# Performance work log

Hardware: AMD Instinct MI355X
Metric: run time of the kernel (lower is better)

Reference implementation:

```python
import jax, jax.numpy as jnp
import numpy as np

TEMPERATURE = 0.07
EPS = 1e-12  # matches torch F.normalize default eps


def setup_inputs() -> dict:
    key = jax.random.key(0)
    k1, k2 = jax.random.split(key)
    N, D = 4096, 768
    z1 = jax.random.normal(k1, (N, D), dtype=jnp.float32)
    z2 = jax.random.normal(k2, (N, D), dtype=jnp.float32)
    return {"z1": z1, "z2": z2}


def reference(z1, z2):
    # L2-normalize each row (torch.F.normalize with eps clamp)
    def l2norm(x):
        n = jnp.linalg.norm(x, axis=1, keepdims=True)
        return x / jnp.maximum(n, EPS)

    z1 = l2norm(z1)
    z2 = l2norm(z2)
    z = jnp.concatenate([z1, z2], axis=0)          # [2N, D]
    N2 = z.shape[0]
    N = N2 // 2

    sim = jnp.matmul(z, z.T) / TEMPERATURE          # [2N, 2N]

    # positive index: row i pairs with i+N (first half) or i-N (second half)
    row_idx = jnp.arange(N2)
    pos_idx = jnp.where(row_idx < N, row_idx + N, row_idx - N)
    pos_vals = sim[row_idx, pos_idx]                # [2N]

    # CE with label 0 over logits [pos, negs] where negs = row minus {self, pos}.
    # logsumexp over {pos} U negs == logsumexp over row with diagonal masked out.
    diag_mask = jnp.eye(N2, dtype=bool)
    sim_no_diag = jnp.where(diag_mask, -jnp.inf, sim)
    lse = jax.nn.logsumexp(sim_no_diag, axis=1)     # [2N]

    loss = jnp.mean(lse - pos_vals)
    return loss
```

## Files before the change

### kernel.cpp

```cpp
#include <hip/hip_runtime.h>
#include <hip/hip_bf16.h>

#define NPAIR 4096
#define DIM   768
#define N2    8192
#define BM    128
#define BNB   128
#define KBLK  128
#define KITER (DIM / KBLK)
#define NSTRIP 16
#define CPB   ((N2 / BNB) / NSTRIP)
#define NBI   (N2 / BM)
#define TOT   (CPB * KITER)
#define SC1   0x7F7F7F7F

constexpr float INV_T = 1.0f / 0.07f;

typedef float f32x16 __attribute__((ext_vector_type(16)));
typedef int   i32x8  __attribute__((ext_vector_type(8)));
#define AS1 __attribute__((address_space(1)))
#define AS3 __attribute__((address_space(3)))

__global__ void knorm(const float* __restrict__ z1, const float* __restrict__ z2,
                      unsigned char* __restrict__ zq, float* __restrict__ rowsum) {
    if (blockIdx.x < 32) rowsum[blockIdx.x * 256 + threadIdx.x] = 0.f;
    const int row  = blockIdx.x * 4 + (threadIdx.x >> 6);
    const int lane = threadIdx.x & 63;
    const float* src = (row < NPAIR) ? (z1 + (size_t)row * DIM)
                                     : (z2 + (size_t)(row - NPAIR) * DIM);
    float4 v[3];
    float ss = 0.f;
#pragma unroll
    for (int i = 0; i < 3; ++i) {
        v[i] = reinterpret_cast<const float4*>(src)[lane + 64 * i];
        ss += v[i].x * v[i].x + v[i].y * v[i].y + v[i].z * v[i].z + v[i].w * v[i].w;
    }
#pragma unroll
    for (int off = 32; off; off >>= 1) ss += __shfl_xor(ss, off);
    const float scale = 1.0f / fmaxf(sqrtf(ss), 1e-12f);
    unsigned int* dst = reinterpret_cast<unsigned int*>(zq + (size_t)row * DIM);
#pragma unroll
    for (int i = 0; i < 3; ++i) {
        unsigned int u = 0;
        u = __builtin_amdgcn_cvt_pk_fp8_f32(v[i].x * scale, v[i].y * scale, u, false);
        u = __builtin_amdgcn_cvt_pk_fp8_f32(v[i].z * scale, v[i].w * scale, u, true);
        dst[lane + 64 * i] = u;
    }
}

__global__ __launch_bounds__(256, 2) void klse(const unsigned char* __restrict__ zq,
                                               float* __restrict__ rowsum,
                                               float* __restrict__ pos) {
    __shared__ __align__(16) unsigned char As[2][BM * KBLK];
    __shared__ __align__(16) unsigned char Bs[2][BM * KBLK];
    const int tid  = threadIdx.x;
    const int wave = tid >> 6;
    const int lane = tid & 63;
    const int wr = wave >> 1, wc = wave & 1;
    const int hi = lane >> 5, rlo = lane & 31;
    const int bi = blockIdx.x;
    const int rb = bi * BM;

    const int sr   = tid >> 3;
    const int soff = (((tid & 7) ^ (sr & 7)) << 4);
    size_t offA[4], offB[4];
#pragma unroll
    for (int i = 0; i < 4; ++i) {
        offA[i] = (size_t)(rb + i * 32 + sr) * DIM + soff;
        offB[i] = (size_t)(i * 32 + sr) * DIM + soff;
    }

    auto stage = [&](int c0, int koff, int buf) {
#pragma unroll
        for (int i = 0; i < 4; ++i) {
            __builtin_amdgcn_global_load_lds(
                (const AS1 unsigned int*)(zq + offA[i] + koff),
                (AS3 unsigned int*)(&As[buf][(i * 256 + tid) * 16]), 16, 0, 0);
            __builtin_amdgcn_global_load_lds(
                (const AS1 unsigned int*)(zq + (size_t)c0 * DIM + offB[i] + koff),
                (AS3 unsigned int*)(&Bs[buf][(i * 256 + tid) * 16]), 16, 0, 0);
        }
    };

    const int sw = rlo & 7;
    int pg[2][2];
#pragma unroll
    for (int s = 0; s < 2; ++s) {
        pg[s][0] = ((4 * s + 2 * hi) ^ sw) << 4;
        pg[s][1] = ((4 * s + 2 * hi + 1) ^ sw) << 4;
    }
    const int raA = (wr * 64 + rlo) * KBLK;
    const int raB = raA + 32 * KBLK;
    const int caA = (wc * 64 + rlo) * KBLK;
    const int caB = caA + 32 * KBLK;

    f32x16 acc00 = {}, acc01 = {}, acc10 = {}, acc11 = {};
    float rowacc0[16], rowacc1[16];
#pragma unroll
    for (int r = 0; r < 16; ++r) { rowacc0[r] = 0.f; rowacc1[r] = 0.f; }
    const int row0b = rb + wr * 64 + 4 * hi;

    stage(blockIdx.y * CPB * BNB, 0, 0);
    asm volatile("s_waitcnt vmcnt(0)" ::: "memory");
    __builtin_amdgcn_s_barrier();

    int ct = 0, kt = 0;
    for (int it = 0; it < TOT; ++it) {
        const int cur = it & 1;
        int nct = ct, nkt = kt + 1;
        if (nkt == KITER) { nkt = 0; ++nct; }
        if (it + 1 < TOT)
            stage((blockIdx.y * CPB + nct) * BNB, nkt * KBLK, cur ^ 1);

#pragma unroll
        for (int s = 0; s < 2; ++s) {
            auto ldf = [&](const unsigned char* p) -> i32x8 {
                int4 u = *reinterpret_cast<const int4*>(p + pg[s][0]);
                int4 v = *reinterpret_cast<const int4*>(p + pg[s][1]);
                return i32x8{u.x, u.y, u.z, u.w, v.x, v.y, v.z, v.w};
            };
            i32x8 a0 = ldf(&As[cur][raA]);
            i32x8 a1 = ldf(&As[cur][raB]);
            i32x8 b0 = ldf(&Bs[cur][caA]);
            i32x8 b1 = ldf(&Bs[cur][caB]);
            acc00 = __builtin_amdgcn_mfma_scale_f32_32x32x64_f8f6f4(a0, b0, acc00, 0, 0, 0, SC1, 0, SC1);
            acc01 = __builtin_amdgcn_mfma_scale_f32_32x32x64_f8f6f4(a0, b1, acc01, 0, 0, 0, SC1, 0, SC1);
            acc10 = __builtin_amdgcn_mfma_scale_f32_32x32x64_f8f6f4(a1, b0, acc10, 0, 0, 0, SC1, 0, SC1);
            acc11 = __builtin_amdgcn_mfma_scale_f32_32x32x64_f8f6f4(a1, b1, acc11, 0, 0, 0, SC1, 0, SC1);
        }

        asm volatile("s_waitcnt vmcnt(0)" ::: "memory");
        __builtin_amdgcn_s_barrier();

        if (kt == KITER - 1) {
            const int cblk = blockIdx.y * CPB + ct;
            const bool on_diag = (cblk == bi);
            const bool on_pos  = (cblk == bi + NPAIR / BNB);
            const int colg = cblk * BNB + wc * 64 + rlo;
#pragma unroll
            for (int r = 0; r < 16; ++r) {
                const int rg0 = row0b + (r & 3) + 8 * (r >> 2);
                float e00 = __expf((acc00[r] - 1.0f) * INV_T);
                float e01 = __expf((acc01[r] - 1.0f) * INV_T);
                float e10 = __expf((acc10[r] - 1.0f) * INV_T);
                float e11 = __expf((acc11[r] - 1.0f) * INV_T);
                if (on_diag) {
                    if (rg0 == colg)           e00 = 0.f;
                    if (rg0 == colg + 32)      e01 = 0.f;
                    if (rg0 + 32 == colg)      e10 = 0.f;
                    if (rg0 + 32 == colg + 32) e11 = 0.f;
                }
                if (on_pos) {
                    if (colg == rg0 + NPAIR)           pos[rg0]      = acc00[r] * INV_T;
                    if (colg + 32 == rg0 + NPAIR)      pos[rg0]      = acc01[r] * INV_T;
                    if (colg == rg0 + 32 + NPAIR)      pos[rg0 + 32] = acc10[r] * INV_T;
                    if (colg + 32 == rg0 + 32 + NPAIR) pos[rg0 + 32] = acc11[r] * INV_T;
                }
                rowacc0[r] += e00 + e01;
                rowacc1[r] += e10 + e11;
            }
            acc00 = f32x16{}; acc01 = f32x16{};
            acc10 = f32x16{}; acc11 = f32x16{};
        }
        ct = nct; kt = nkt;
    }

#pragma unroll
    for (int r = 0; r < 16; ++r) {
#pragma unroll
        for (int m = 1; m < 32; m <<= 1) {
            rowacc0[r] += __shfl_xor(rowacc0[r], m);
            rowacc1[r] += __shfl_xor(rowacc1[r], m);
        }
    }
    if (rlo == 0) {
#pragma unroll
        for (int r = 0; r < 16; ++r) {
            const int rg0 = row0b + (r & 3) + 8 * (r >> 2);
            atomicAdd(&rowsum[rg0], rowacc0[r]);
            atomicAdd(&rowsum[rg0 + 32], rowacc1[r]);
        }
    }
}

__global__ void kfinal(const float* __restrict__ rowsum, const float* __restrict__ pos,
                       float* __restrict__ out) {
    __shared__ float red[8];
    const int tid = threadIdx.x;
    float s = 0.f;
    for (int i = tid; i < N2; i += 512) {
        const int p = (i < NPAIR) ? i : i - NPAIR;
        s += INV_T + __logf(rowsum[i]) - pos[p];
    }
#pragma unroll
    for (int off = 32; off; off >>= 1) s += __shfl_xor(s, off);
    if ((tid & 63) == 0) red[tid >> 6] = s;
    __syncthreads();
    if (tid == 0) {
        float t = 0.f;
#pragma unroll
        for (int w = 0; w < 8; ++w) t += red[w];
        out[0] = t / (float)N2;
    }
}

extern "C" void kernel_launch(void* const* d_in, const int* in_sizes, int n_in,
                              void* d_out, int out_size, void* d_ws, size_t ws_size,
                              hipStream_t stream) {
    const float* z1 = (const float*)d_in[0];
    const float* z2 = (const float*)d_in[1];
    unsigned char* zq = (unsigned char*)d_ws;
    float* rowsum = (float*)((char*)d_ws + (size_t)N2 * DIM);
    float* pos = rowsum + N2;
    float* out = (float*)d_out;

    hipLaunchKernelGGL(knorm, dim3(N2 / 4), dim3(256), 0, stream, z1, z2, zq, rowsum);
    hipLaunchKernelGGL(klse, dim3(NBI, NSTRIP), dim3(256), 0, stream, zq, rowsum, pos);
    hipLaunchKernelGGL(kfinal, dim3(1), dim3(512), 0, stream, rowsum, pos, out);
}
```

Baseline: 88.53 us.

## Widen column tile to 256 and halve K block for more MFMA reuse

Each block now covers 256 columns instead of 128, while the K step drops from 128 to 64. Each wave holds a 2x4 grid of 32x32 accumulators rather than 2x2, so every A fragment loaded from LDS feeds four MFMAs. The LDS swizzle and staging addressing are rewritten for the 64-byte row width, and the diagonal and positive-pair detection now compares against bi>>1. This is meant to cut LDS and global traffic per MFMA, at the cost of more accumulator registers and twice as many barrier-synchronised iterations per tile.

```diff
diff --git a/kernel.cpp b/kernel.cpp
--- a/kernel.cpp
+++ b/kernel.cpp
@@ -5,8 +5,8 @@
 #define DIM   768
 #define N2    8192
 #define BM    128
-#define BNB   128
-#define KBLK  128
+#define BNB   256
+#define KBLK  64
 #define KITER (DIM / KBLK)
 #define NSTRIP 16
 #define CPB   ((N2 / BNB) / NSTRIP)
@@ -52,7 +52,7 @@
                                                float* __restrict__ rowsum,
                                                float* __restrict__ pos) {
     __shared__ __align__(16) unsigned char As[2][BM * KBLK];
-    __shared__ __align__(16) unsigned char Bs[2][BM * KBLK];
+    __shared__ __align__(16) unsigned char Bs[2][BNB * KBLK];
     const int tid  = threadIdx.x;
     const int wave = tid >> 6;
     const int lane = tid & 63;
@@ -61,40 +61,54 @@
     const int bi = blockIdx.x;
     const int rb = bi * BM;
 
-    const int sr   = tid >> 3;
-    const int soff = (((tid & 7) ^ (sr & 7)) << 4);
-    size_t offA[4], offB[4];
+    size_t offA[2]; int dstA[2];
+#pragma unroll
+    for (int i = 0; i < 2; ++i) {
+        const int g = i * 256 + tid, r = g >> 2, s = g & 3;
+        offA[i] = (size_t)(rb + r) * DIM + ((s ^ ((r >> 1) & 3)) << 4);
+        dstA[i] = g * 16;
+    }
+    size_t offB[4]; int dstB[4];
 #pragma unroll
     for (int i = 0; i < 4; ++i) {
-        offA[i] = (size_t)(rb + i * 32 + sr) * DIM + soff;
-        offB[i] = (size_t)(i * 32 + sr) * DIM + soff;
+        const int g = i * 256 + tid, r = g >> 2, s = g & 3;
+        offB[i] = (size_t)r * DIM + ((s ^ ((r >> 1) & 3)) << 4);
+        dstB[i] = g * 16;
     }
 
     auto stage = [&](int c0, int koff, int buf) {
 #pragma unroll
-        for (int i = 0; i < 4; ++i) {
+        for (int i = 0; i < 2; ++i)
             __builtin_amdgcn_global_load_lds(
                 (const AS1 unsigned int*)(zq + offA[i] + koff),
-                (AS3 unsigned int*)(&As[buf][(i * 256 + tid) * 16]), 16, 0, 0);
+                (AS3 unsigned int*)(&As[buf][dstA[i]]), 16, 0, 0);
+#pragma unroll
+        for (int i = 0; i < 4; ++i)
             __builtin_amdgcn_global_load_lds(
                 (const AS1 unsigned int*)(zq + (size_t)c0 * DIM + offB[i] + koff),
-                (AS3 unsigned int*)(&Bs[buf][(i * 256 + tid) * 16]), 16, 0, 0);
-        }
+                (AS3 unsigned int*)(&Bs[buf][dstB[i]]), 16, 0, 0);
     };
 
-    const int sw = rlo & 7;
-    int pg[2][2];
-#pragma unroll
-    for (int s = 0; s < 2; ++s) {
-        pg[s][0] = ((4 * s + 2 * hi) ^ sw) << 4;
-        pg[s][1] = ((4 * s + 2 * hi + 1) ^ sw) << 4;
-    }
-    const int raA = (wr * 64 + rlo) * KBLK;
-    const int raB = raA + 32 * KBLK;
-    const int caA = (wc * 64 + rlo) * KBLK;
-    const int caB = caA + 32 * KBLK;
-
-    f32x16 acc00 = {}, acc01 = {}, acc10 = {}, acc11 = {};
+    const int sw  = (rlo >> 1) & 3;
+    const int pg0 = ((2 * hi) ^ sw) << 4;
+    const int pg1 = ((2 * hi + 1) ^ sw) << 4;
+    int raOff[2], cbOff[4];
+#pragma unroll
+    for (int m = 0; m < 2; ++m) raOff[m] = (wr * 64 + m * 32 + rlo) * KBLK;
+#pragma unroll
+    for (int n = 0; n < 4; ++n) cbOff[n] = (wc * 128 + n * 32 + rlo) * KBLK;
+
+    auto ldf = [&](const unsigned char* p) -> i32x8 {
+        int4 u = *reinterpret_cast<const int4*>(p + pg0);
+        int4 v = *reinterpret_cast<const int4*>(p + pg1);
+        return i32x8{u.x, u.y, u.z, u.w, v.x, v.y, v.z, v.w};
+    };
+
+    f32x16 acc[2][4];
+#pragma unroll
+    for (int m = 0; m < 2; ++m)
+#pragma unroll
+        for (int n = 0; n < 4; ++n) acc[m][n] = f32x16{};
     float rowacc0[16], rowacc1[16];
 #pragma unroll
     for (int r = 0; r < 16; ++r) { rowacc0[r] = 0.f; rowacc1[r] = 0.f; }
@@ -112,55 +126,56 @@
         if (it + 1 < TOT)
             stage((blockIdx.y * CPB + nct) * BNB, nkt * KBLK, cur ^ 1);
 
-#pragma unroll
-        for (int s = 0; s < 2; ++s) {
-            auto ldf = [&](const unsigned char* p) -> i32x8 {
-                int4 u = *reinterpret_cast<const int4*>(p + pg[s][0]);
-                int4 v = *reinterpret_cast<const int4*>(p + pg[s][1]);
-                return i32x8{u.x, u.y, u.z, u.w, v.x, v.y, v.z, v.w};
-            };
-            i32x8 a0 = ldf(&As[cur][raA]);
-            i32x8 a1 = ldf(&As[cur][raB]);
-            i32x8 b0 = ldf(&Bs[cur][caA]);
-            i32x8 b1 = ldf(&Bs[cur][caB]);
-            acc00 = __builtin_amdgcn_mfma_scale_f32_32x32x64_f8f6f4(a0, b0, acc00, 0, 0, 0, SC1, 0, SC1);
-            acc01 = __builtin_amdgcn_mfma_scale_f32_32x32x64_f8f6f4(a0, b1, acc01, 0, 0, 0, SC1, 0, SC1);
-            acc10 = __builtin_amdgcn_mfma_scale_f32_32x32x64_f8f6f4(a1, b0, acc10, 0, 0, 0, SC1, 0, SC1);
-            acc11 = __builtin_amdgcn_mfma_scale_f32_32x32x64_f8f6f4(a1, b1, acc11, 0, 0, 0, SC1, 0, SC1);
-        }
+        i32x8 a0 = ldf(&As[cur][raOff[0]]);
+        i32x8 a1 = ldf(&As[cur][raOff[1]]);
+        i32x8 b0 = ldf(&Bs[cur][cbOff[0]]);
+        i32x8 b1 = ldf(&Bs[cur][cbOff[1]]);
+        i32x8 b2 = ldf(&Bs[cur][cbOff[2]]);
+        i32x8 b3 = ldf(&Bs[cur][cbOff[3]]);
+        acc[0][0] = __builtin_amdgcn_mfma_scale_f32_32x32x64_f8f6f4(a0, b0, acc[0][0], 0, 0, 0, SC1, 0, SC1);
+        acc[0][1] = __builtin_amdgcn_mfma_scale_f32_32x32x64_f8f6f4(a0, b1, acc[0][1], 0, 0, 0, SC1, 0, SC1);
+        acc[0][2] = __builtin_amdgcn_mfma_scale_f32_32x32x64_f8f6f4(a0, b2, acc[0][2], 0, 0, 0, SC1, 0, SC1);
+        acc[0][3] = __builtin_amdgcn_mfma_scale_f32_32x32x64_f8f6f4(a0, b3, acc[0][3], 0, 0, 0, SC1, 0, SC1);
+        acc[1][0] = __builtin_amdgcn_mfma_scale_f32_32x32x64_f8f6f4(a1, b0, acc[1][0], 0, 0, 0, SC1, 0, SC1);
+        acc[1][1] = __builtin_amdgcn_mfma_scale_f32_32x32x64_f8f6f4(a1, b1, acc[1][1], 0, 0, 0, SC1, 0, SC1);
+        acc[1][2] = __builtin_amdgcn_mfma_scale_f32_32x32x64_f8f6f4(a1, b2, acc[1][2], 0, 0, 0, SC1, 0, SC1);
+        acc[1][3] = __builtin_amdgcn_mfma_scale_f32_32x32x64_f8f6f4(a1, b3, acc[1][3], 0, 0, 0, SC1, 0, SC1);
 
         asm volatile("s_waitcnt vmcnt(0)" ::: "memory");
         __builtin_amdgcn_s_barrier();
 
         if (kt == KITER - 1) {
-            const int cblk = blockIdx.y * CPB + ct;
-            const bool on_diag = (cblk == bi);
-            const bool on_pos  = (cblk == bi + NPAIR / BNB);
-            const int colg = cblk * BNB + wc * 64 + rlo;
+            const int cb = blockIdx.y * CPB + ct;
+            const bool on_diag = (cb == (bi >> 1));
+            const bool on_pos  = (cb == (bi >> 1) + NPAIR / BNB);
 #pragma unroll
             for (int r = 0; r < 16; ++r) {
                 const int rg0 = row0b + (r & 3) + 8 * (r >> 2);
-                float e00 = __expf((acc00[r] - 1.0f) * INV_T);
-                float e01 = __expf((acc01[r] - 1.0f) * INV_T);
-                float e10 = __expf((acc10[r] - 1.0f) * INV_T);
-                float e11 = __expf((acc11[r] - 1.0f) * INV_T);
-                if (on_diag) {
-                    if (rg0 == colg)           e00 = 0.f;
-                    if (rg0 == colg + 32)      e01 = 0.f;
-                    if (rg0 + 32 == colg)      e10 = 0.f;
-                    if (rg0 + 32 == colg + 32) e11 = 0.f;
+                const int rg1 = rg0 + 32;
+                float s0 = 0.f, s1 = 0.f;
+#pragma unroll
+                for (int n = 0; n < 4; ++n) {
+                    const int colg = cb * BNB + wc * 128 + n * 32 + rlo;
+                    float e0 = __expf((acc[0][n][r] - 1.0f) * INV_T);
+                    float e1 = __expf((acc[1][n][r] - 1.0f) * INV_T);
+                    if (on_diag) {
+                        if (rg0 == colg) e0 = 0.f;
+                        if (rg1 == colg) e1 = 0.f;
+                    }
+                    if (on_pos) {
+                        if (colg == rg0 + NPAIR) pos[rg0] = acc[0][n][r] * INV_T;
+                        if (colg == rg1 + NPAIR) pos[rg1] = acc[1][n][r] * INV_T;
+                    }
+                    s0 += e0;
+                    s1 += e1;
                 }
-                if (on_pos) {
-                    if (colg == rg0 + NPAIR)           pos[rg0]      = acc00[r] * INV_T;
-                    if (colg + 32 == rg0 + NPAIR)      pos[rg0]      = acc01[r] * INV_T;
-                    if (colg == rg0 + 32 + NPAIR)      pos[rg0 + 32] = acc10[r] * INV_T;
-                    if (colg + 32 == rg0 + 32 + NPAIR) pos[rg0 + 32] = acc11[r] * INV_T;
-                }
-                rowacc0[r] += e00 + e01;
-                rowacc1[r] += e10 + e11;
+                rowacc0[r] += s0;
+                rowacc1[r] += s1;
             }
-            acc00 = f32x16{}; acc01 = f32x16{};
-            acc10 = f32x16{}; acc11 = f32x16{};
+#pragma unroll
+            for (int m = 0; m < 2; ++m)
+#pragma unroll
+                for (int n = 0; n < 4; ++n) acc[m][n] = f32x16{};
         }
         ct = nct; kt = nkt;
     }
```

Result: slower. 110.0 us (+24.3%).
